# Optimization experiments

Measured on AMD Instinct MI355X. Metric: run time of the kernel, lower is better.

The kernel has to match this reference:

```python
import jax, jax.numpy as jnp
import numpy as np

B, L = 8, 2048
H_IN = 20
K1, K2 = 16, 32
NG = 32            # n_gaussians
D1, D2 = 7, 5      # gaussian kernel input dims
DM = 128           # outer product out_features
DH = 32            # attribute embedding out_features
IDX_MAX = 8.0      # index_distance_max


def _gather(x, idx):
    # x: (B,L,H), idx: (B,L,K) -> (B,L,K,H)
    b = jnp.arange(x.shape[0])[:, None, None]
    return x[b, idx]


def _neighbors(frames, kmax):
    c = frames[:, :, 0, :]                      # centers (B,L,3)
    sq = jnp.sum(c * c, axis=-1)
    d2 = sq[:, :, None] + sq[:, None, :] - 2.0 * jnp.einsum('bld,bmd->blm', c, c)
    _, idx = jax.lax.top_k(-d2, kmax)           # self (d2=0) lands in slot 0
    return idx


def _coords(frames, seq_idx, idx):
    c = frames[:, :, 0, :]
    axes = frames[:, :, 1:4, :]                 # local frame axes of center node
    z = frames[:, :, 3, :]
    c_j = _gather(c, idx)
    z_j = _gather(z, idx)
    delta = c_j - c[:, :, None, :]              # (B,L,K,3)
    dist = jnp.sqrt(jnp.sum(delta * delta, -1, keepdims=True) + 1e-12)
    eucl = jnp.einsum('blkd,blad->blka', delta, axes)   # neighbor coords in local frame
    zdotz = jnp.sum(z[:, :, None, :] * z_j, -1, keepdims=True)
    deltadotz = jnp.sum(delta * z_j, -1, keepdims=True) / dist
    zdotdelta = jnp.sum(z[:, :, None, :] * delta, -1, keepdims=True) / dist
    sidx = seq_idx.astype(jnp.float32)          # (B,L,1)
    idist = jnp.clip(jnp.abs(_gather(sidx, idx) - sidx[:, :, None, :]), 0.0, IDX_MAX)
    return eucl, dist, zdotz, deltadotz, zdotdelta, idist


def _gaussian(x, centers, prec):
    # full-covariance Gaussian kernel: exp(-0.5 ||P_n (x - mu_n)||^2)
    diff = x[..., None] - centers               # (...,d,NG)
    y = jnp.einsum('...dn,dkn->...kn', diff, prec)
    return jnp.exp(-0.5 * jnp.sum(y * y, axis=-2))


def _forward(aa_attributes, aa_frame, aa_indices,
             gk1_centers, gk1_prec, op_kernel, op_bias,
             emb_W, emb_b, beta_W, beta_b, selfatt_W, selfatt_b,
             crossatt_W, crossatt_b, nodef_W, nodef_b,
             gk2_centers, gk2_prec, emb2_W, emb2_b):
    # --- neighborhood 1: euclidian + index_distance + ZdotZ + (DeltadotZ,ZdotDelta)
    idx1 = _neighbors(aa_frame, K1)
    eucl, _, zz, dz, zd, idist = _coords(aa_frame, aa_indices, idx1)
    coords1 = jnp.concatenate([eucl, idist, zz, dz, zd], axis=-1)   # (B,L,K1,7)
    neigh_attr = _gather(aa_attributes, idx1)                        # (B,L,K1,20)
    g1 = _gaussian(coords1, gk1_centers, gk1_prec)                   # (B,L,K1,NG)
    # outer-product embedding: sum over neighbors and (gaussian x attribute) pairs
    filt = jnp.einsum('blkg,blkh,gho->blo', g1, neigh_attr, op_kernel) + op_bias
    f = jax.nn.relu(filt)                                            # (B,L,128)
    emb = jax.nn.relu(f @ emb_W + emb_b)                             # (B,L,32)
    beta = jax.nn.relu(emb @ beta_W + beta_b)                        # (B,L,1)
    satt = jax.nn.relu(emb @ selfatt_W + selfatt_b)                  # (B,L,1)
    catt = jax.nn.relu(emb @ crossatt_W + crossatt_b)                # (B,L,1)
    nodef = jax.nn.relu(emb @ nodef_W + nodef_b)                     # (B,L,2)
    # --- neighborhood 2: distance + ZdotZ + (DeltadotZ,ZdotDelta) + index_distance
    idx2 = _neighbors(aa_frame, K2)
    _, dist2, zz2, dz2, zd2, idist2 = _coords(aa_frame, aa_indices, idx2)
    coords2 = jnp.concatenate([dist2, zz2, dz2, zd2, idist2], axis=-1)  # (B,L,K2,5)
    att_local = _gather(catt, idx2)                                  # (B,L,K2,1)
    nodef_local = _gather(nodef, idx2)                               # (B,L,K2,2)
    g2 = _gaussian(coords2, gk2_centers, gk2_prec)                   # (B,L,K2,NG)
    gw = jax.nn.relu(g2 @ emb2_W + emb2_b)                           # (B,L,K2,1)
    # --- graph attention aggregation (self slot is k=0)
    e = att_local.at[:, :, 0, :].set(satt)
    logits = beta[:, :, None, :] * e
    logits = logits - jnp.max(logits, axis=2, keepdims=True)
    w = gw * jnp.exp(logits)
    a = w / (jnp.sum(w, axis=2, keepdims=True) + 1e-6)               # (B,L,K2,1)
    out = jnp.sum(a * nodef_local, axis=2)                           # (B,L,2)
    return out


def setup_inputs():
    key = jax.random.key(0)
    ks = jax.random.split(key, 16)
    eye1 = jnp.tile(jnp.eye(D1, dtype=jnp.float32)[:, :, None], (1, 1, NG))
    eye2 = jnp.tile(jnp.eye(D2, dtype=jnp.float32)[:, :, None], (1, 1, NG))
    return {
        'aa_attributes': jax.random.normal(ks[0], (B, L, H_IN), jnp.float32),
        'aa_frame': jax.random.normal(ks[1], (B, L, 4, 3), jnp.float32),
        'aa_indices': jnp.arange(B * L, dtype=jnp.int32).reshape(B, L, 1),
        'gk1_centers': 0.1 * jax.random.normal(ks[2], (D1, NG), jnp.float32),
        'gk1_prec': eye1 + 0.05 * jax.random.normal(ks[3], (D1, D1, NG), jnp.float32),
        'op_kernel': 0.05 * jax.random.normal(ks[4], (NG, H_IN, DM), jnp.float32),
        'op_bias': jnp.zeros((DM,), jnp.float32),
        'emb_W': jax.random.normal(ks[5], (DM, DH), jnp.float32) / np.sqrt(DM),
        'emb_b': jnp.zeros((DH,), jnp.float32),
        'beta_W': jax.random.normal(ks[6], (DH, 1), jnp.float32) / np.sqrt(DH),
        'beta_b': jnp.zeros((1,), jnp.float32),
        'selfatt_W': jax.random.normal(ks[7], (DH, 1), jnp.float32) / np.sqrt(DH),
        'selfatt_b': jnp.zeros((1,), jnp.float32),
        'crossatt_W': jax.random.normal(ks[8], (DH, 1), jnp.float32) / np.sqrt(DH),
        'crossatt_b': jnp.zeros((1,), jnp.float32),
        'nodef_W': jax.random.normal(ks[9], (DH, 2), jnp.float32) / np.sqrt(DH),
        'nodef_b': jnp.zeros((2,), jnp.float32),
        'gk2_centers': 0.1 * jax.random.normal(ks[10], (D2, NG), jnp.float32),
        'gk2_prec': eye2 + 0.05 * jax.random.normal(ks[11], (D2, D2, NG), jnp.float32),
        'emb2_W': jax.random.normal(ks[12], (NG, 1), jnp.float32) / np.sqrt(NG),
        'emb2_b': jnp.zeros((1,), jnp.float32),
    }


def reference(aa_attributes, aa_frame, aa_indices,
              gk1_centers, gk1_prec, op_kernel, op_bias,
              emb_W, emb_b, beta_W, beta_b, selfatt_W, selfatt_b,
              crossatt_W, crossatt_b, nodef_W, nodef_b,
              gk2_centers, gk2_prec, emb2_W, emb2_b):
    return _forward(aa_attributes, aa_frame, aa_indices,
                    gk1_centers, gk1_prec, op_kernel, op_bias,
                    emb_W, emb_b, beta_W, beta_b, selfatt_W, selfatt_b,
                    crossatt_W, crossatt_b, nodef_W, nodef_b,
                    gk2_centers, gk2_prec, emb2_W, emb2_b)
```

## Files before the change

### kernel.cpp

```cpp
#include <hip/hip_runtime.h>

typedef unsigned int u32;
typedef unsigned long long u64;
typedef unsigned short u16;

#define NL 2048

typedef __attribute__((ext_vector_type(8))) short bf16x8;
typedef __attribute__((ext_vector_type(16))) float f32x16;

__device__ __forceinline__ u16 to_bf16(float f) {
  u32 b = __float_as_uint(f);
  b += 0x7FFFu + ((b >> 16) & 1u);
  return (u16)(b >> 16);
}

__device__ __forceinline__ void gload_lds16(const void* g, void* l) {
  __builtin_amdgcn_global_load_lds(
      (const __attribute__((address_space(1))) u32*)g,
      (__attribute__((address_space(3))) u32*)l, 16, 0, 0);
}

__device__ __forceinline__ u64 shfl_xor64(u64 v, int m) {
  int lo = __shfl_xor((int)(u32)v, m, 64);
  int hi = __shfl_xor((int)(u32)(v >> 32), m, 64);
  return ((u64)(u32)hi << 32) | (u32)lo;
}

__device__ __forceinline__ u32 sort64_u32(u32 v, int lane) {
#pragma unroll
  for (int k = 2; k <= 64; k <<= 1) {
#pragma unroll
    for (int j = k >> 1; j > 0; j >>= 1) {
      u32 p = (u32)__shfl_xor((int)v, j, 64);
      bool lower = ((lane & j) == 0);
      bool asc = ((lane & k) == 0);
      u32 lo = v < p ? v : p;
      u32 hi = v < p ? p : v;
      v = (lower == asc) ? lo : hi;
    }
  }
  return v;
}

__device__ __forceinline__ u64 sort64_u64(u64 v, int lane) {
#pragma unroll
  for (int k = 2; k <= 64; k <<= 1) {
#pragma unroll
    for (int j = k >> 1; j > 0; j >>= 1) {
      u64 p = shfl_xor64(v, j);
      bool lower = ((lane & j) == 0);
      bool asc = ((lane & k) == 0);
      u64 lo = v < p ? v : p;
      u64 hi = v < p ? p : v;
      v = (lower == asc) ? lo : hi;
    }
  }
  return v;
}

__global__ __launch_bounds__(512) void knn_prep_kernel(
    const float* __restrict__ frames, int* __restrict__ idx32,
    const float* __restrict__ opW, const float* __restrict__ embW,
    const float* __restrict__ betaW, const float* __restrict__ sattW,
    const float* __restrict__ cattW, const float* __restrict__ nodW,
    const float* __restrict__ betaB, const float* __restrict__ sattB,
    const float* __restrict__ cattB, const float* __restrict__ nodB,
    u16* __restrict__ opWt, u16* __restrict__ embWt, float* __restrict__ w5,
    float* __restrict__ b5) {
  __shared__ union U {
    struct {
      float4 cand[2048];
      u64 comp[8][256];
    } k;
    float tp[128 * 73];
  } sm;
  const int bx = blockIdx.x;
  const int tid = threadIdx.x;

  if (bx >= 2048) {
    if (bx < 2058) {
      const int k0 = (bx - 2048) * 64;
#pragma unroll
      for (int j = 0; j < 4; j++) {
        int f = tid + j * 512;
        int kk = f >> 5;
        int o4 = (f & 31) * 4;
        float4 v = *(const float4*)(opW + (size_t)(k0 + kk) * 128 + o4);
        sm.tp[(o4 + 0) * 73 + kk] = v.x;
        sm.tp[(o4 + 1) * 73 + kk] = v.y;
        sm.tp[(o4 + 2) * 73 + kk] = v.z;
        sm.tp[(o4 + 3) * 73 + kk] = v.w;
      }
      __syncthreads();
      u32* ow = (u32*)opWt;
#pragma unroll
      for (int j = 0; j < 8; j++) {
        int f = tid + j * 512;
        int o = f >> 5, q = f & 31;
        float lo = sm.tp[o * 73 + q * 2];
        float hi = sm.tp[o * 73 + q * 2 + 1];
        ow[o * 320 + (k0 >> 1) + q] = (u32)to_bf16(lo) | ((u32)to_bf16(hi) << 16);
      }
    } else {
      for (int f = tid; f < 4096; f += 512) {
        int j = f >> 7, kk = f & 127;
        embWt[f] = to_bf16(embW[(size_t)kk * 32 + j]);
      }
      if (tid < 160) {
        int h = tid >> 5, j = tid & 31;
        float v = (h == 0) ? betaW[j]
                  : (h == 1) ? sattW[j]
                  : (h == 2) ? cattW[j]
                  : (h == 3) ? nodW[j * 2]
                             : nodW[j * 2 + 1];
        w5[j * 8 + h] = v;
      } else if (tid < 165) {
        int h = tid - 160;
        float v = (h == 0) ? betaB[0]
                  : (h == 1) ? sattB[0]
                  : (h == 2) ? cattB[0]
                  : (h == 3) ? nodB[0]
                             : nodB[1];
        b5[h] = v;
      }
    }
    return;
  }

  const int w = tid >> 6, lane = tid & 63;
  const int query = bx * 8 + w;
  const int b = query >> 11, lq = query & (NL - 1);

#pragma unroll
  for (int i = 0; i < 4; i++) {
    int l = tid + i * 512;
    const float* fp = frames + (size_t)(b * NL + l) * 12;
    float4 fr = *(const float4*)fp;
    sm.k.cand[l] = make_float4(fr.x, fr.y, fr.z,
                               fr.x * fr.x + fr.y * fr.y + fr.z * fr.z);
  }
  __syncthreads();

  float4 me = sm.k.cand[lq];
  u32 k[32];
  u32 m = 0xFFFFFFFFu;
#pragma unroll
  for (int i = 0; i < 32; i++) {
    float4 c = sm.k.cand[i * 64 + lane];
    float dot = c.x * me.x + c.y * me.y + c.z * me.z;
    float d2 = (me.w + c.w) - 2.0f * dot;
    u32 kb = __float_as_uint(d2);
    u32 key = kb ^ ((u32)((int)kb >> 31) | 0x80000000u);
    k[i] = key;
    m = key < m ? key : m;
  }

  u32 ms = sort64_u32(m, lane);
  u32 T0 = (u32)__shfl((int)ms, 31, 64);

  int base = 0;
#pragma unroll
  for (int i = 0; i < 32; i++) {
    bool flag = (k[i] <= T0);
    u64 mask = __ballot(flag);
    if (flag) {
      u32 rank = __builtin_amdgcn_mbcnt_hi(
          (u32)(mask >> 32), __builtin_amdgcn_mbcnt_lo((u32)mask, 0u));
      int pos = base + (int)rank;
      if (pos < 256) sm.k.comp[w][pos] = ((u64)k[i] << 32) | (u32)(i * 64 + lane);
    }
    base += (int)__popcll(mask);
  }
  int cnt = base < 256 ? base : 256;
  __syncthreads();

  if (cnt <= 64) {
    int pz = cnt + lane;
    if (pz < 64) sm.k.comp[w][pz] = ~0ull;
    u64 e0 = sm.k.comp[w][lane];
    u64 s = sort64_u64(e0, lane);
    if (lane < 32)
      idx32[(size_t)query * 32 + lane] = (int)(s & 0xFFFFFFFFull);
  } else {
    for (int b0 = 0; b0 < cnt; b0 += 64) {
      bool live = (b0 + lane < cnt);
      u64 e = live ? sm.k.comp[w][b0 + lane] : ~0ull;
      int r = 0;
      for (int mi = 0; mi < cnt; mi++) {
        u64 em = sm.k.comp[w][mi];
        r += (em < e) ? 1 : 0;
      }
      if (live && r < 32)
        idx32[(size_t)query * 32 + r] = (int)(e & 0xFFFFFFFFull);
    }
  }
}

__global__ __launch_bounds__(256) void stage1_kernel(
    const float* __restrict__ frames, const float* __restrict__ attrs,
    const int* __restrict__ aaidx, const float* __restrict__ cen1,
    const float* __restrict__ prec1, const int* __restrict__ idx32,
    u16* __restrict__ outer) {
  __shared__ float sCoord[4 * 16 * 8];
  __shared__ float sAttrT[4 * 20 * 16];
  __shared__ float sG1T[4 * 32 * 17];
  const int tid = threadIdx.x;
  const int pt = tid >> 6, lane = tid & 63;
  const int pid = blockIdx.x * 4 + pt;
  const int b = pid >> 11;
  const int g = lane & 31;

  float pr[7][7], cn[7];
#pragma unroll
  for (int d = 0; d < 7; d++) {
    cn[d] = cen1[d * 32 + g];
#pragma unroll
    for (int kk = 0; kk < 7; kk++) pr[d][kk] = prec1[(d * 7 + kk) * 32 + g];
  }

  {
    const int nn = lane >> 2, q = lane & 3;
    int j2 = idx32[pid * 32 + nn];
    int jg2 = b * NL + j2;
    const float* ar = attrs + (size_t)jg2 * 20;
    float4 v = *(const float4*)(ar + q * 4);
    float* aw = sAttrT + pt * 320 + nn;
    aw[(q * 4 + 0) * 16] = v.x;
    aw[(q * 4 + 1) * 16] = v.y;
    aw[(q * 4 + 2) * 16] = v.z;
    aw[(q * 4 + 3) * 16] = v.w;
    if (q == 3) {
      float4 v4 = *(const float4*)(ar + 16);
      aw[16 * 16] = v4.x;
      aw[17 * 16] = v4.y;
      aw[18 * 16] = v4.z;
      aw[19 * 16] = v4.w;
    }
  }

  if (lane < 16) {
    int n = lane;
    int j = idx32[pid * 32 + n];
    int jg = b * NL + j;
    const float* fs = frames + (size_t)pid * 12;
    const float* fj = frames + (size_t)jg * 12;
    float4 A0 = *(const float4*)(fs);
    float4 A1 = *(const float4*)(fs + 4);
    float4 A2 = *(const float4*)(fs + 8);
    float4 B0 = *(const float4*)(fj);
    float4 B2 = *(const float4*)(fj + 8);
    float dx = B0.x - A0.x, dy = B0.y - A0.y, dzc = B0.z - A0.z;
    float a0x = A0.w, a0y = A1.x, a0z = A1.y;
    float a1x = A1.z, a1y = A1.w, a1z = A2.x;
    float a2x = A2.y, a2y = A2.z, a2z = A2.w;
    float zjx = B2.y, zjy = B2.z, zjz = B2.w;
    float dd = dx * dx + dy * dy + dzc * dzc + 1e-12f;
    float dist = sqrtf(dd);
    float e0 = dx * a0x + dy * a0y + dzc * a0z;
    float e1 = dx * a1x + dy * a1y + dzc * a1z;
    float e2 = dx * a2x + dy * a2y + dzc * a2z;
    float zz = a2x * zjx + a2y * zjy + a2z * zjz;
    float dzv = (dx * zjx + dy * zjy + dzc * zjz) / dist;
    float zdv = (a2x * dx + a2y * dy + a2z * dzc) / dist;
    float si = (float)aaidx[pid];
    float sj = (float)aaidx[jg];
    float idist = fminf(fabsf(sj - si), 8.0f);
    float* cr = sCoord + pt * 128 + n * 8;
    cr[0] = e0; cr[1] = e1; cr[2] = e2; cr[3] = idist;
    cr[4] = zz; cr[5] = dzv; cr[6] = zdv;
  }
  __syncthreads();
  {
    const int nh = lane >> 5;
#pragma unroll
    for (int i = 0; i < 8; i++) {
      int n = nh * 8 + i;
      const float* cr = sCoord + pt * 128 + n * 8;
      float df[7];
#pragma unroll
      for (int d = 0; d < 7; d++) df[d] = cr[d] - cn[d];
      float s = 0.0f;
#pragma unroll
      for (int kk = 0; kk < 7; kk++) {
        float y = 0.0f;
#pragma unroll
        for (int d = 0; d < 7; d++) y = fmaf(df[d], pr[d][kk], y);
        s = fmaf(y, y, s);
      }
      sG1T[pt * 544 + g * 17 + n] = __expf(-0.5f * s);
    }
  }
  __syncthreads();
  {
    const int hg = lane >> 5;
    float g16[16];
#pragma unroll
    for (int n = 0; n < 16; n++) g16[n] = sG1T[pt * 544 + g * 17 + n];
    u32* orow = (u32*)(outer + (size_t)pid * 640) + (g * 20 + hg * 10) / 2;
#pragma unroll
    for (int i = 0; i < 5; i++) {
      int h0 = hg * 10 + i * 2, h1 = h0 + 1;
      float a0 = 0.f, a1 = 0.f;
#pragma unroll
      for (int c = 0; c < 4; c++) {
        float4 v0 = *(float4*)&sAttrT[pt * 320 + h0 * 16 + c * 4];
        float4 v1 = *(float4*)&sAttrT[pt * 320 + h1 * 16 + c * 4];
        a0 = fmaf(v0.x, g16[c * 4 + 0], a0);
        a0 = fmaf(v0.y, g16[c * 4 + 1], a0);
        a0 = fmaf(v0.z, g16[c * 4 + 2], a0);
        a0 = fmaf(v0.w, g16[c * 4 + 3], a0);
        a1 = fmaf(v1.x, g16[c * 4 + 0], a1);
        a1 = fmaf(v1.y, g16[c * 4 + 1], a1);
        a1 = fmaf(v1.z, g16[c * 4 + 2], a1);
        a1 = fmaf(v1.w, g16[c * 4 + 3], a1);
      }
      orow[i] = (u32)to_bf16(a0) | ((u32)to_bf16(a1) << 16);
    }
  }
}

__global__ __launch_bounds__(256) void gemm_kernel(
    const u16* __restrict__ outer,
    const u16* __restrict__ opWt,
    const float* __restrict__ opB,
    const u16* __restrict__ embWt,
    const float* __restrict__ embB,
    const float* __restrict__ w5,
    const float* __restrict__ b5,
    float* __restrict__ head8) {
  __shared__ char smem[40960];
  const int tid = threadIdx.x;
  const int w = tid >> 6, lane = tid & 63;
  const int p0 = blockIdx.x * 32;
  const int lr = lane >> 3, lc = lane & 7;
  const int gsw = lc ^ lr;
  const int m = lane & 31, kh = lane >> 5;

  f32x16 acc;
#pragma unroll
  for (int r = 0; r < 16; r++) acc[r] = 0.f;

  const u16* gA = outer + (size_t)(p0 + w * 8 + lr) * 640 + gsw * 8;
#pragma unroll
  for (int cc = 0; cc < 10; cc++)
    gload_lds16(gA + cc * 64, smem + cc * 4096 + w * 1024);
  __syncthreads();

  const u16* gB = opWt + (size_t)(w * 32 + m) * 640;
#pragma unroll
  for (int cc = 0; cc < 10; cc++) {
#pragma unroll
    for (int s = 0; s < 4; s++) {
      int pg = (s * 2 + kh) ^ (m & 7);
      bf16x8 av = *(bf16x8*)(smem + cc * 4096 + m * 128 + pg * 16);
      bf16x8 bv = *(const bf16x8*)(gB + cc * 64 + s * 16 + kh * 8);
      acc = __builtin_amdgcn_mfma_f32_32x32x16_bf16(av, bv, acc, 0, 0, 0);
    }
  }
  __syncthreads();

  const int o = w * 32 + m;
  float bo = opB[o];
#pragma unroll
  for (int i = 0; i < 2; i++) {
    int j = w * 8 + i * 4 + (lane >> 4);
    int ge = (lane & 15) ^ (j & 7);
    gload_lds16(embWt + j * 128 + ge * 8, smem + 8192 + w * 2048 + i * 1024);
  }
  u16* sFb = (u16*)smem;
#pragma unroll
  for (int r = 0; r < 16; r++) {
    int mm = (r & 3) + 8 * (r >> 2) + 4 * kh;
    float v = fmaxf(acc[r] + bo, 0.f);
    int pg = (o >> 3) ^ (mm & 7);
    sFb[mm * 128 + pg * 8 + (o & 7)] = to_bf16(v);
  }
  __syncthreads();

  f32x16 acc2;
#pragma unroll
  for (int r = 0; r < 16; r++) acc2[r] = 0.f;
#pragma unroll
  for (int t2 = 0; t2 < 2; t2++) {
    int gg = (w * 2 + t2) * 2 + kh;
    int pg = gg ^ (m & 7);
    bf16x8 av = *(bf16x8*)(smem + m * 256 + pg * 16);
    bf16x8 bv = *(bf16x8*)(smem + 8192 + m * 256 + pg * 16);
    acc2 = __builtin_amdgcn_mfma_f32_32x32x16_bf16(av, bv, acc2, 0, 0, 0);
  }
  float* scr = (float*)(smem + 16384) + w * 1024;
#pragma unroll
  for (int r = 0; r < 16; r++) {
    int mm = (r & 3) + 8 * (r >> 2) + 4 * kh;
    scr[mm * 32 + m] = acc2[r];
  }
  __syncthreads();

  {
    float* sc = (float*)(smem + 16384);
    int i4 = tid * 4;
    float4 v0 = *(float4*)(sc + i4);
    float4 v1 = *(float4*)(sc + 1024 + i4);
    float4 v2 = *(float4*)(sc + 2048 + i4);
    float4 v3 = *(float4*)(sc + 3072 + i4);
    int pp = tid >> 3, j0 = (tid & 7) * 4;
    float4 eb = *(const float4*)(embB + j0);
    float4 e;
    e.x = fmaxf(v0.x + v1.x + v2.x + v3.x + eb.x, 0.f);
    e.y = fmaxf(v0.y + v1.y + v2.y + v3.y + eb.y, 0.f);
    e.z = fmaxf(v0.z + v1.z + v2.z + v3.z + eb.z, 0.f);
    e.w = fmaxf(v0.w + v1.w + v2.w + v3.w + eb.w, 0.f);
    *(float4*)((float*)smem + pp * 36 + j0) = e;
  }
  __syncthreads();

  if (tid < 160) {
    int h = tid >> 5, p = tid & 31;
    const float* sE = (const float*)smem + p * 36;
    float a = b5[h];
#pragma unroll
    for (int j = 0; j < 32; j++) a = fmaf(sE[j], w5[j * 8 + h], a);
    a = fmaxf(a, 0.f);
    int slot = (h < 2) ? (h + 4) : (h - 2);
    head8[(size_t)(p0 + p) * 8 + slot] = a;
  }
}

__global__ __launch_bounds__(256) void stage2_kernel(
    const float* __restrict__ frames, const int* __restrict__ aaidx,
    const float* __restrict__ cen2, const float* __restrict__ prec2,
    const float* __restrict__ emb2W, const float* __restrict__ emb2B,
    const int* __restrict__ idx32, const float* __restrict__ head8,
    float* __restrict__ out) {
  __shared__ float sCoord[8 * 32 * 5];
  __shared__ float sG2[8 * 32 * 33];
  const int tid = threadIdx.x;
  const int pt = tid >> 5, n = tid & 31;
  const int pid = blockIdx.x * 8 + pt;
  const int b = pid >> 11;
  const int g = n;

  float pr[5][5], cn[5];
#pragma unroll
  for (int d = 0; d < 5; d++) {
    cn[d] = cen2[d * 32 + g];
#pragma unroll
    for (int kk = 0; kk < 5; kk++) pr[d][kk] = prec2[(d * 5 + kk) * 32 + g];
  }

  float4 hv;
  float betaS, sattS;
  {
    int j = idx32[pid * 32 + n];
    int jg = b * NL + j;
    const float* fs = frames + (size_t)pid * 12;
    const float* fj = frames + (size_t)jg * 12;
    float4 A0 = *(const float4*)(fs);
    float4 A2 = *(const float4*)(fs + 8);
    float4 B0 = *(const float4*)(fj);
    float4 B2 = *(const float4*)(fj + 8);
    float dx = B0.x - A0.x, dy = B0.y - A0.y, dzc = B0.z - A0.z;
    float a2x = A2.y, a2y = A2.z, a2z = A2.w;
    float zjx = B2.y, zjy = B2.z, zjz = B2.w;
    float dd = dx * dx + dy * dy + dzc * dzc + 1e-12f;
    float dist = sqrtf(dd);
    float zz = a2x * zjx + a2y * zjy + a2z * zjz;
    float dzv = (dx * zjx + dy * zjy + dzc * zjz) / dist;
    float zdv = (a2x * dx + a2y * dy + a2z * dzc) / dist;
    float si = (float)aaidx[pid];
    float sj = (float)aaidx[jg];
    float idist = fminf(fabsf(sj - si), 8.0f);
    float* cr = sCoord + pt * 160 + n * 5;
    cr[0] = dist; cr[1] = zz; cr[2] = dzv; cr[3] = zdv; cr[4] = idist;
    hv = *(const float4*)(head8 + (size_t)jg * 8);
    betaS = head8[(size_t)pid * 8 + 4];
    sattS = head8[(size_t)pid * 8 + 5];
  }
  __syncthreads();
  {
#pragma unroll 8
    for (int i = 0; i < 32; i++) {
      const float* cr = sCoord + pt * 160 + i * 5;
      float df[5];
#pragma unroll
      for (int d = 0; d < 5; d++) df[d] = cr[d] - cn[d];
      float s = 0.0f;
#pragma unroll
      for (int kk = 0; kk < 5; kk++) {
        float y = 0.0f;
#pragma unroll
        for (int d = 0; d < 5; d++) y = fmaf(df[d], pr[d][kk], y);
        s = fmaf(y, y, s);
      }
      sG2[pt * 1056 + i * 33 + g] = __expf(-0.5f * s);
    }
  }
  __syncthreads();
  {
    float gw = emb2B[0];
#pragma unroll 8
    for (int gg = 0; gg < 32; gg++)
      gw = fmaf(sG2[pt * 1056 + n * 33 + gg], emb2W[gg], gw);
    gw = fmaxf(gw, 0.0f);
    float e = (n == 0) ? sattS : hv.x;
    float logit = betaS * e;
    float mx = logit;
#pragma unroll
    for (int d = 1; d < 32; d <<= 1) mx = fmaxf(mx, __shfl_xor(mx, d, 64));
    float wv = gw * __expf(logit - mx);
    float S = wv;
#pragma unroll
    for (int d = 1; d < 32; d <<= 1) S += __shfl_xor(S, d, 64);
    float a = wv / (S + 1e-6f);
    float o0 = a * hv.y, o1 = a * hv.z;
#pragma unroll
    for (int d = 1; d < 32; d <<= 1) {
      o0 += __shfl_xor(o0, d, 64);
      o1 += __shfl_xor(o1, d, 64);
    }
    if (n == 0) {
      out[pid * 2 + 0] = o0;
      out[pid * 2 + 1] = o1;
    }
  }
}

extern "C" void kernel_launch(void* const* d_in, const int* in_sizes, int n_in,
                              void* d_out, int out_size, void* d_ws, size_t ws_size,
                              hipStream_t stream) {
  const float* attrs = (const float*)d_in[0];
  const float* frames = (const float*)d_in[1];
  const int* aaidx = (const int*)d_in[2];
  const float* cen1 = (const float*)d_in[3];
  const float* prec1 = (const float*)d_in[4];
  const float* opW = (const float*)d_in[5];
  const float* opB = (const float*)d_in[6];
  const float* embW = (const float*)d_in[7];
  const float* embB = (const float*)d_in[8];
  const float* betaW = (const float*)d_in[9];
  const float* betaB = (const float*)d_in[10];
  const float* sattW = (const float*)d_in[11];
  const float* sattB = (const float*)d_in[12];
  const float* cattW = (const float*)d_in[13];
  const float* cattB = (const float*)d_in[14];
  const float* nodW = (const float*)d_in[15];
  const float* nodB = (const float*)d_in[16];
  const float* cen2 = (const float*)d_in[17];
  const float* prec2 = (const float*)d_in[18];
  const float* emb2W = (const float*)d_in[19];
  const float* emb2B = (const float*)d_in[20];
  float* out = (float*)d_out;

  char* ws = (char*)d_ws;
  int* idx32 = (int*)ws;
  u16* outer_bf = (u16*)(ws + 2097152);
  float* head8 = (float*)(ws + 23068672);
  u16* opWt = (u16*)(ws + 23592960);
  u16* embWt = (u16*)(ws + 23756800);
  float* w5 = (float*)(ws + 23764992);
  float* b5 = (float*)(ws + 23766016);

  knn_prep_kernel<<<dim3(2059), dim3(512), 0, stream>>>(
      frames, idx32, opW, embW, betaW, sattW, cattW, nodW, betaB, sattB,
      cattB, nodB, opWt, embWt, w5, b5);
  stage1_kernel<<<dim3(4096), dim3(256), 0, stream>>>(frames, attrs, aaidx, cen1,
                                                      prec1, idx32, outer_bf);
  gemm_kernel<<<dim3(512), dim3(256), 0, stream>>>(outer_bf, opWt, opB, embWt,
                                                   embB, w5, b5, head8);
  stage2_kernel<<<dim3(2048), dim3(256), 0, stream>>>(frames, aaidx, cen2, prec2,
                                                      emb2W, emb2B, idx32, head8, out);
}
```

Measured before the change: 185.7 us.

## Fuse stage1 neighborhood featurization into the kNN kernel

Merges the stage1 kernel into the kNN/prep kernel. Each wave now consumes its freshly computed neighbor indices from LDS instead of re-reading idx32 from global memory, and the separate launch goes away. Gaussian values are exchanged between half-waves with a lane shuffle instead of an LDS transpose buffer plus barrier. The cost is more register pressure and LDS use in a 512-thread block, and the parameter loads for the Gaussian now run inside the kNN block.

```diff
diff --git a/kernel.cpp b/kernel.cpp
--- a/kernel.cpp
+++ b/kernel.cpp
@@ -59,8 +59,11 @@
   return v;
 }
 
-__global__ __launch_bounds__(512) void knn_prep_kernel(
-    const float* __restrict__ frames, int* __restrict__ idx32,
+__global__ __launch_bounds__(512) void knn_s1_prep_kernel(
+    const float* __restrict__ frames, const float* __restrict__ attrs,
+    const int* __restrict__ aaidx, const float* __restrict__ cen1,
+    const float* __restrict__ prec1, int* __restrict__ idx32,
+    u16* __restrict__ outer,
     const float* __restrict__ opW, const float* __restrict__ embW,
     const float* __restrict__ betaW, const float* __restrict__ sattW,
     const float* __restrict__ cattW, const float* __restrict__ nodW,
@@ -132,6 +135,11 @@
   const int query = bx * 8 + w;
   const int b = query >> 11, lq = query & (NL - 1);
 
+  char* wb = (char*)&sm + 32768 + w * 1920;
+  float* sCoord = (float*)wb;
+  float* sAttrT = sCoord + 128;
+  u32* idxw = (u32*)(sAttrT + 320);
+
 #pragma unroll
   for (int i = 0; i < 4; i++) {
     int l = tid + i * 512;
@@ -180,8 +188,11 @@
     if (pz < 64) sm.k.comp[w][pz] = ~0ull;
     u64 e0 = sm.k.comp[w][lane];
     u64 s = sort64_u64(e0, lane);
-    if (lane < 32)
-      idx32[(size_t)query * 32 + lane] = (int)(s & 0xFFFFFFFFull);
+    if (lane < 32) {
+      u32 jn = (u32)(s & 0xFFFFFFFFull);
+      idx32[(size_t)query * 32 + lane] = (int)jn;
+      idxw[lane] = jn;
+    }
   } else {
     for (int b0 = 0; b0 < cnt; b0 += 64) {
       bool live = (b0 + lane < cnt);
@@ -191,41 +202,24 @@
         u64 em = sm.k.comp[w][mi];
         r += (em < e) ? 1 : 0;
       }
-      if (live && r < 32)
-        idx32[(size_t)query * 32 + r] = (int)(e & 0xFFFFFFFFull);
-    }
-  }
-}
-
-__global__ __launch_bounds__(256) void stage1_kernel(
-    const float* __restrict__ frames, const float* __restrict__ attrs,
-    const int* __restrict__ aaidx, const float* __restrict__ cen1,
-    const float* __restrict__ prec1, const int* __restrict__ idx32,
-    u16* __restrict__ outer) {
-  __shared__ float sCoord[4 * 16 * 8];
-  __shared__ float sAttrT[4 * 20 * 16];
-  __shared__ float sG1T[4 * 32 * 17];
-  const int tid = threadIdx.x;
-  const int pt = tid >> 6, lane = tid & 63;
-  const int pid = blockIdx.x * 4 + pt;
-  const int b = pid >> 11;
-  const int g = lane & 31;
-
-  float pr[7][7], cn[7];
-#pragma unroll
-  for (int d = 0; d < 7; d++) {
-    cn[d] = cen1[d * 32 + g];
-#pragma unroll
-    for (int kk = 0; kk < 7; kk++) pr[d][kk] = prec1[(d * 7 + kk) * 32 + g];
-  }
+      if (live && r < 32) {
+        u32 jn = (u32)(e & 0xFFFFFFFFull);
+        idx32[(size_t)query * 32 + r] = (int)jn;
+        idxw[r] = jn;
+      }
+    }
+  }
+  __syncthreads();
+
+  const int pid = query;
+  const int g = lane & 31, nh = lane >> 5;
 
   {
     const int nn = lane >> 2, q = lane & 3;
-    int j2 = idx32[pid * 32 + nn];
-    int jg2 = b * NL + j2;
+    int jg2 = b * NL + (int)idxw[nn];
     const float* ar = attrs + (size_t)jg2 * 20;
     float4 v = *(const float4*)(ar + q * 4);
-    float* aw = sAttrT + pt * 320 + nn;
+    float* aw = sAttrT + nn;
     aw[(q * 4 + 0) * 16] = v.x;
     aw[(q * 4 + 1) * 16] = v.y;
     aw[(q * 4 + 2) * 16] = v.z;
@@ -238,11 +232,9 @@
       aw[19 * 16] = v4.w;
     }
   }
-
   if (lane < 16) {
     int n = lane;
-    int j = idx32[pid * 32 + n];
-    int jg = b * NL + j;
+    int jg = b * NL + (int)idxw[n];
     const float* fs = frames + (size_t)pid * 12;
     const float* fj = frames + (size_t)jg * 12;
     float4 A0 = *(const float4*)(fs);
@@ -266,17 +258,26 @@
     float si = (float)aaidx[pid];
     float sj = (float)aaidx[jg];
     float idist = fminf(fabsf(sj - si), 8.0f);
-    float* cr = sCoord + pt * 128 + n * 8;
+    float* cr = sCoord + n * 8;
     cr[0] = e0; cr[1] = e1; cr[2] = e2; cr[3] = idist;
     cr[4] = zz; cr[5] = dzv; cr[6] = zdv;
   }
   __syncthreads();
-  {
-    const int nh = lane >> 5;
+
+  float g16[16];
+  {
+    float pr[7][7], cn[7];
+#pragma unroll
+    for (int d = 0; d < 7; d++) {
+      cn[d] = cen1[d * 32 + g];
+#pragma unroll
+      for (int kk = 0; kk < 7; kk++) pr[d][kk] = prec1[(d * 7 + kk) * 32 + g];
+    }
+    float gv[8];
 #pragma unroll
     for (int i = 0; i < 8; i++) {
       int n = nh * 8 + i;
-      const float* cr = sCoord + pt * 128 + n * 8;
+      const float* cr = sCoord + n * 8;
       float df[7];
 #pragma unroll
       for (int d = 0; d < 7; d++) df[d] = cr[d] - cn[d];
@@ -288,15 +289,18 @@
         for (int d = 0; d < 7; d++) y = fmaf(df[d], pr[d][kk], y);
         s = fmaf(y, y, s);
       }
-      sG1T[pt * 544 + g * 17 + n] = __expf(-0.5f * s);
-    }
-  }
-  __syncthreads();
-  {
-    const int hg = lane >> 5;
-    float g16[16];
-#pragma unroll
-    for (int n = 0; n < 16; n++) g16[n] = sG1T[pt * 544 + g * 17 + n];
+      gv[i] = __expf(-0.5f * s);
+    }
+#pragma unroll
+    for (int i = 0; i < 8; i++) {
+      float ov = __shfl_xor(gv[i], 32, 64);
+      g16[i] = nh ? ov : gv[i];
+      g16[8 + i] = nh ? gv[i] : ov;
+    }
+  }
+
+  {
+    const int hg = nh;
     u32* orow = (u32*)(outer + (size_t)pid * 640) + (g * 20 + hg * 10) / 2;
 #pragma unroll
     for (int i = 0; i < 5; i++) {
@@ -304,8 +308,8 @@
       float a0 = 0.f, a1 = 0.f;
 #pragma unroll
       for (int c = 0; c < 4; c++) {
-        float4 v0 = *(float4*)&sAttrT[pt * 320 + h0 * 16 + c * 4];
-        float4 v1 = *(float4*)&sAttrT[pt * 320 + h1 * 16 + c * 4];
+        float4 v0 = *(float4*)&sAttrT[h0 * 16 + c * 4];
+        float4 v1 = *(float4*)&sAttrT[h1 * 16 + c * 4];
         a0 = fmaf(v0.x, g16[c * 4 + 0], a0);
         a0 = fmaf(v0.y, g16[c * 4 + 1], a0);
         a0 = fmaf(v0.z, g16[c * 4 + 2], a0);
@@ -561,11 +565,9 @@
   float* w5 = (float*)(ws + 23764992);
   float* b5 = (float*)(ws + 23766016);
 
-  knn_prep_kernel<<<dim3(2059), dim3(512), 0, stream>>>(
-      frames, idx32, opW, embW, betaW, sattW, cattW, nodW, betaB, sattB,
-      cattB, nodB, opWt, embWt, w5, b5);
-  stage1_kernel<<<dim3(4096), dim3(256), 0, stream>>>(frames, attrs, aaidx, cen1,
-                                                      prec1, idx32, outer_bf);
+  knn_s1_prep_kernel<<<dim3(2059), dim3(512), 0, stream>>>(
+      frames, attrs, aaidx, cen1, prec1, idx32, outer_bf, opW, embW, betaW,
+      sattW, cattW, nodW, betaB, sattB, cattB, nodB, opWt, embWt, w5, b5);
   gemm_kernel<<<dim3(512), dim3(256), 0, stream>>>(outer_bf, opWt, opB, embWt,
                                                    embB, w5, b5, head8);
   stage2_kernel<<<dim3(2048), dim3(256), 0, stream>>>(frames, aaidx, cen2, prec2,
```

Measured after the change: 184.3 us. About the same (-0.7%).
